# Kernel optimization log

Measured on AMD Instinct MI355X. Metric: run time of the kernel, lower is better.

The kernel has to match this reference:

```python
import jax, jax.numpy as jnp
import numpy as np

B, IN_DIM, HID, LAT, L, K = 65536, 512, 256, 64, 3, 2048


def setup_inputs() -> dict:
    key = jax.random.key(0)
    ks = jax.random.split(key, 10)
    s = 0.05
    return {
        "x": jax.random.normal(ks[0], (B, IN_DIM), jnp.float32),
        "enc_w1": jax.random.normal(ks[1], (IN_DIM, HID), jnp.float32) * s,
        "enc_b1": jnp.zeros((HID,), jnp.float32),
        "enc_w2": jax.random.normal(ks[2], (HID, LAT), jnp.float32) * s,
        "enc_b2": jnp.zeros((LAT,), jnp.float32),
        "codebooks": jax.random.normal(ks[3], (L, K, LAT), jnp.float32),
        "dec_w1": jax.random.normal(ks[4], (LAT, HID), jnp.float32) * s,
        "dec_b1": jnp.zeros((HID,), jnp.float32),
        "dec_w2": jax.random.normal(ks[5], (HID, IN_DIM), jnp.float32) * s,
        "dec_b2": jnp.zeros((IN_DIM,), jnp.float32),
    }


def reference(x, enc_w1, enc_b1, enc_w2, enc_b2, codebooks,
              dec_w1, dec_b1, dec_w2, dec_b2):
    # encoder: Linear -> ReLU -> Linear
    z = jax.nn.relu(x @ enc_w1 + enc_b1) @ enc_w2 + enc_b2  # [B, LAT]

    quantized = jnp.zeros_like(z)
    codes, residuals = [], []
    num_layers = codebooks.shape[0]
    for i in range(num_layers):  # small fixed layer loop (structurally sequential)
        residual = z - jax.lax.stop_gradient(quantized)  # [B, LAT]
        residuals.append(residual)
        C = codebooks[i]  # [K, LAT]
        # squared euclidean distances (argmin identical to cdist argmin)
        sqdist = (jnp.sum(residual * residual, axis=-1, keepdims=True)
                  - 2.0 * (residual @ C.T)
                  + jnp.sum(C * C, axis=-1))  # [B, K]
        code = jnp.argmin(sqdist, axis=-1)  # [B]
        codes.append(code)
        quantized = C[code] + jax.lax.stop_gradient(quantized)

    # decoder: Linear -> ReLU -> Linear
    x_recon = jax.nn.relu(quantized @ dec_w1 + dec_b1) @ dec_w2 + dec_b2  # [B, IN_DIM]
    return (jnp.stack(codes), x_recon, quantized, jnp.stack(residuals))
```

## Files before the change

### kernel.cpp

```cpp
#include <hip/hip_runtime.h>
#include <float.h>

#define NB      65536
#define IN_DIM  512
#define HID     256
#define LAT     64
#define NLAYERS 3
#define NK      2048
#define DELTA   1e-2f

typedef __attribute__((ext_vector_type(8)))  short s16x8;
typedef __attribute__((ext_vector_type(16))) float fp32x16;

__device__ __forceinline__ unsigned short f2bf(float v) {
  unsigned u = __float_as_uint(v);
  unsigned r = (u + 0x7fffu + ((u >> 16) & 1u)) >> 16;
  return (unsigned short)r;
}
__device__ __forceinline__ float bf2f(unsigned short h) {
  return __uint_as_float((unsigned)h << 16);
}

template<bool RELU>
__global__ __launch_bounds__(256) void gemm_f32(
    const float* __restrict__ A, const float* __restrict__ W,
    const float* __restrict__ bias, float* __restrict__ C,
    int M, int N, int K) {
  __shared__ float As[32][132];
  __shared__ float Bs[32][64];
  const int tid = threadIdx.x;
  const int cg  = tid & 15;
  const int rg  = tid >> 4;
  const int m0  = blockIdx.x * 128;
  const int n0  = blockIdx.y * 64;

  float acc[8][4];
#pragma unroll
  for (int i = 0; i < 8; ++i)
#pragma unroll
    for (int j = 0; j < 4; ++j) acc[i][j] = 0.f;

  for (int k0 = 0; k0 < K; k0 += 32) {
#pragma unroll
    for (int p = 0; p < 4; ++p) {
      int a = tid + p * 256;
      int row = a >> 3, kq = (a & 7) * 4;
      float4 v = *reinterpret_cast<const float4*>(&A[(size_t)(m0 + row) * K + k0 + kq]);
      As[kq + 0][row] = v.x; As[kq + 1][row] = v.y;
      As[kq + 2][row] = v.z; As[kq + 3][row] = v.w;
    }
#pragma unroll
    for (int p = 0; p < 2; ++p) {
      int a = tid + p * 256;
      int kk = a >> 4, nq = (a & 15) * 4;
      *reinterpret_cast<float4*>(&Bs[kk][nq]) =
          *reinterpret_cast<const float4*>(&W[(size_t)(k0 + kk) * N + n0 + nq]);
    }
    __syncthreads();
#pragma unroll
    for (int kk = 0; kk < 32; ++kk) {
      float4 a0 = *reinterpret_cast<const float4*>(&As[kk][rg * 8]);
      float4 a1 = *reinterpret_cast<const float4*>(&As[kk][rg * 8 + 4]);
      float4 b0 = *reinterpret_cast<const float4*>(&Bs[kk][cg * 4]);
      float av[8] = {a0.x, a0.y, a0.z, a0.w, a1.x, a1.y, a1.z, a1.w};
      float bv[4] = {b0.x, b0.y, b0.z, b0.w};
#pragma unroll
      for (int i = 0; i < 8; ++i)
#pragma unroll
        for (int j = 0; j < 4; ++j)
          acc[i][j] = fmaf(av[i], bv[j], acc[i][j]);
    }
    __syncthreads();
  }

  float4 bb = *reinterpret_cast<const float4*>(&bias[n0 + cg * 4]);
  float bv[4] = {bb.x, bb.y, bb.z, bb.w};
#pragma unroll
  for (int i = 0; i < 8; ++i) {
    float vals[4];
#pragma unroll
    for (int j = 0; j < 4; ++j) {
      float v = __fadd_rn(acc[i][j], bv[j]);
      if (RELU) v = fmaxf(v, 0.f);
      vals[j] = v;
    }
    float4 o; o.x = vals[0]; o.y = vals[1]; o.z = vals[2]; o.w = vals[3];
    *reinterpret_cast<float4*>(&C[(size_t)(m0 + rg * 8 + i) * N + n0 + cg * 4]) = o;
  }
}

template<bool RELU>
__global__ __launch_bounds__(256) void gemm128(
    const float* __restrict__ A, const float* __restrict__ W,
    const float* __restrict__ bias, float* __restrict__ C,
    int M, int N, int K) {
  __shared__ float As[16][132];
  __shared__ float Bs[16][132];
  const int tid  = threadIdx.x;
  const int cg   = tid & 15;
  const int rg   = tid >> 4;
  const int sw   = (cg >> 2) & 1;
  const int colA = cg * 8 + sw * 4;
  const int colB = cg * 8 + (sw ^ 1) * 4;
  const int m0   = blockIdx.x * 128;
  const int n0   = blockIdx.y * 128;

  const int arow = tid >> 2;
  const int akq  = (tid & 3) * 4;
  const int bk   = tid >> 5;
  const int bn   = (tid & 31) * 4;

  const float* Ap0 = A + (size_t)(m0 + arow) * K + akq;
  const float* Ap1 = A + (size_t)(m0 + arow + 64) * K + akq;
  const float* Wp0 = W + (size_t)bk * N + n0 + bn;
  const float* Wp1 = W + (size_t)(bk + 8) * N + n0 + bn;

  float acc[8][8];
#pragma unroll
  for (int i = 0; i < 8; ++i)
#pragma unroll
    for (int j = 0; j < 8; ++j) acc[i][j] = 0.f;

  float4 av0, av1, bv0, bv1;
  av0 = *reinterpret_cast<const float4*>(Ap0);
  av1 = *reinterpret_cast<const float4*>(Ap1);
  bv0 = *reinterpret_cast<const float4*>(Wp0);
  bv1 = *reinterpret_cast<const float4*>(Wp1);

  auto write_tile = [&]() {
    As[akq + 0][arow] = av0.x; As[akq + 1][arow] = av0.y;
    As[akq + 2][arow] = av0.z; As[akq + 3][arow] = av0.w;
    As[akq + 0][arow + 64] = av1.x; As[akq + 1][arow + 64] = av1.y;
    As[akq + 2][arow + 64] = av1.z; As[akq + 3][arow + 64] = av1.w;
    *reinterpret_cast<float4*>(&Bs[bk][bn])     = bv0;
    *reinterpret_cast<float4*>(&Bs[bk + 8][bn]) = bv1;
  };
  auto compute_tile = [&]() {
#pragma unroll
    for (int kk = 0; kk < 16; ++kk) {
      float4 a0 = *reinterpret_cast<const float4*>(&As[kk][rg * 8]);
      float4 a1 = *reinterpret_cast<const float4*>(&As[kk][rg * 8 + 4]);
      float4 b0 = *reinterpret_cast<const float4*>(&Bs[kk][colA]);
      float4 b1 = *reinterpret_cast<const float4*>(&Bs[kk][colB]);
      float rv[8] = {a0.x, a0.y, a0.z, a0.w, a1.x, a1.y, a1.z, a1.w};
      float cv[8] = {b0.x, b0.y, b0.z, b0.w, b1.x, b1.y, b1.z, b1.w};
#pragma unroll
      for (int i = 0; i < 8; ++i)
#pragma unroll
        for (int j = 0; j < 8; ++j)
          acc[i][j] = fmaf(rv[i], cv[j], acc[i][j]);
    }
  };

  write_tile();
  __syncthreads();
#pragma unroll 1
  for (int k0 = 16; k0 < K; k0 += 16) {
    av0 = *reinterpret_cast<const float4*>(Ap0 + k0);
    av1 = *reinterpret_cast<const float4*>(Ap1 + k0);
    bv0 = *reinterpret_cast<const float4*>(Wp0 + (size_t)k0 * N);
    bv1 = *reinterpret_cast<const float4*>(Wp1 + (size_t)k0 * N);
    compute_tile();
    __syncthreads();
    write_tile();
    __syncthreads();
  }
  compute_tile();

  float4 bA = *reinterpret_cast<const float4*>(&bias[n0 + colA]);
  float4 bB = *reinterpret_cast<const float4*>(&bias[n0 + colB]);
  float ba[8] = {bA.x, bA.y, bA.z, bA.w, bB.x, bB.y, bB.z, bB.w};
#pragma unroll
  for (int i = 0; i < 8; ++i) {
    size_t row = (size_t)(m0 + rg * 8 + i);
    float o[8];
#pragma unroll
    for (int j = 0; j < 8; ++j) {
      float v = __fadd_rn(acc[i][j], ba[j]);
      if (RELU) v = fmaxf(v, 0.f);
      o[j] = v;
    }
    float4 oA; oA.x = o[0]; oA.y = o[1]; oA.z = o[2]; oA.w = o[3];
    float4 oB; oB.x = o[4]; oB.y = o[5]; oB.z = o[6]; oB.w = o[7];
    *reinterpret_cast<float4*>(&C[row * N + n0 + colA]) = oA;
    *reinterpret_cast<float4*>(&C[row * N + n0 + colB]) = oB;
  }
}

__global__ void cnorm_f32(const float* __restrict__ cb, float* __restrict__ cn) {
  int i = blockIdx.x * blockDim.x + threadIdx.x;
  if (i >= NLAYERS * NK) return;
  const float* row = cb + (size_t)i * LAT;
  float r[8];
#pragma unroll
  for (int j = 0; j < 8; ++j) r[j] = 0.f;
#pragma unroll
  for (int t = 0; t < 8; ++t)
#pragma unroll
    for (int j = 0; j < 8; ++j) {
      float v = row[t * 8 + j];
      r[j] = __fadd_rn(r[j], __fmul_rn(v, v));
    }
  cn[i] = __fadd_rn(__fadd_rn(__fadd_rn(r[0], r[1]), __fadd_rn(r[2], r[3])),
                    __fadd_rn(__fadd_rn(r[4], r[5]), __fadd_rn(r[6], r[7])));
}

__global__ void split_cb(const float* __restrict__ cb,
                         unsigned short* __restrict__ cbf) {
  const int sid  = blockIdx.x * 256 + threadIdx.x;
  const int lane = sid & 63;
  const int grp  = sid >> 6;
  const int fg   = grp & 7;
  const int chl  = grp >> 3;
  const int nt = fg >> 2, ks = fg & 3;
  const int layer = chl >> 5, ch = chl & 31;
  const int code = ch * 64 + nt * 32 + (lane & 31);
  const int k0 = ks * 16 + (lane >> 5) * 8;
  const float* src = cb + ((size_t)layer * NK + code) * LAT + k0;
  float4 a = *(const float4*)src;
  float4 b = *(const float4*)(src + 4);
  float v[8] = {a.x, a.y, a.z, a.w, b.x, b.y, b.z, b.w};
  s16x8 hi, lo;
#pragma unroll
  for (int i = 0; i < 8; ++i) {
    unsigned short h = f2bf(v[i]);
    hi[i] = (short)h;
    lo[i] = (short)f2bf(__fsub_rn(v[i], bf2f(h)));
  }
  *(s16x8*)(cbf + ((size_t)grp * 2 + 0) * 512 + lane * 8) = hi;
  *(s16x8*)(cbf + ((size_t)grp * 2 + 1) * 512 + lane * 8) = lo;
}

__global__ void split_w(const float* __restrict__ W,
                        unsigned short* __restrict__ wf, int K, int N) {
  const int total = (K / 16) * (N / 32) * 64;
  const int idx = blockIdx.x * 256 + threadIdx.x;
  if (idx >= total) return;
  const int lane = idx & 63;
  const int grp  = idx >> 6;
  const int ntn  = N / 32;
  const int ks   = grp / ntn;
  const int ntg  = grp % ntn;
  const int col  = ntg * 32 + (lane & 31);
  const int k0   = ks * 16 + (lane >> 5) * 8;
  s16x8 hi, lo;
#pragma unroll
  for (int i = 0; i < 8; ++i) {
    float v = W[(size_t)(k0 + i) * N + col];
    unsigned short h = f2bf(v);
    hi[i] = (short)h;
    lo[i] = (short)f2bf(__fsub_rn(v, bf2f(h)));
  }
  *(s16x8*)(wf + ((size_t)grp * 2 + 0) * 512 + lane * 8) = hi;
  *(s16x8*)(wf + ((size_t)grp * 2 + 1) * 512 + lane * 8) = lo;
}

__global__ __launch_bounds__(256, 2) void rq_mfma(
    const float* __restrict__ zg,
    const float* __restrict__ cb,
    const unsigned short* __restrict__ cbf,
    const float* __restrict__ cnorm,
    float* __restrict__ out_codes,
    float* __restrict__ out_quant,
    float* __restrict__ out_res) {
  __shared__ unsigned short cbS[2][8192];
  __shared__ float cnSL[NK];
  __shared__ float m1S[128][2];
  __shared__ int   candS[128][8];
  __shared__ int   cntS[128][2];
  __shared__ int   flagS[128][2];
  __shared__ int   selS[128];
  __shared__ float rnS[128];
  __shared__ float bestD[256];
  __shared__ int   bestK[256];

  const int tid    = threadIdx.x;
  const int w      = tid >> 6;
  const int rgrp   = w >> 1;
  const int nthalf = w & 1;
  const int lane   = tid & 63;
  const int half   = lane >> 5;
  const int lcol   = lane & 31;
  const int rb0    = blockIdx.x * 128;

  s16x8 ah[2][4], al[2][4];

  for (int layer = 0; layer < NLAYERS; ++layer) {
    const float* cbL = cb + (size_t)layer * NK * LAT;
    const float* cnL = cnorm + (size_t)layer * NK;
    const unsigned short* cbfL = cbf + (size_t)layer * (NK * LAT * 2);
    float* resL = out_res + (size_t)layer * NB * LAT;

#pragma unroll
    for (int m = 0; m < 2; ++m) {
      const size_t row = (size_t)(rb0 + rgrp * 64 + m * 32 + lcol);
#pragma unroll
      for (int ks = 0; ks < 4; ++ks) {
        const int k0 = ks * 16 + half * 8;
        const float* zp = zg + row * LAT + k0;
        float4 a = *(const float4*)zp;
        float4 b = *(const float4*)(zp + 4);
        float r[8] = {a.x, a.y, a.z, a.w, b.x, b.y, b.z, b.w};
        if (layer > 0) {
          const float* qp = out_quant + row * LAT + k0;
          float4 qa = *(const float4*)qp;
          float4 qb = *(const float4*)(qp + 4);
          float q[8] = {qa.x, qa.y, qa.z, qa.w, qb.x, qb.y, qb.z, qb.w};
#pragma unroll
          for (int i = 0; i < 8; ++i) r[i] = __fsub_rn(r[i], q[i]);
          if (nthalf == 0) {
            float4 o0 = {r[0], r[1], r[2], r[3]};
            float4 o1 = {r[4], r[5], r[6], r[7]};
            *(float4*)(resL + row * LAT + k0) = o0;
            *(float4*)(resL + row * LAT + k0 + 4) = o1;
          }
        }
#pragma unroll
        for (int i = 0; i < 8; ++i) {
          unsigned short hh = f2bf(r[i]);
          float hf = bf2f(hh);
          ah[m][ks][i] = (short)hh;
          al[m][ks][i] = (short)f2bf(__fsub_rn(r[i], hf));
        }
      }
    }

    s16x8 stg[4];
#pragma unroll
    for (int p = 0; p < 4; ++p)
      stg[p] = *(const s16x8*)(cbfL + p * 2048 + tid * 8);
    float4 cn0 = *(const float4*)(cnL + tid * 8);
    float4 cn1 = *(const float4*)(cnL + tid * 8 + 4);
    __syncthreads();

#pragma unroll
    for (int p = 0; p < 4; ++p)
      *(s16x8*)(&cbS[0][p * 2048 + tid * 8]) = stg[p];
    *(float4*)(&cnSL[tid * 8])     = cn0;
    *(float4*)(&cnSL[tid * 8 + 4]) = cn1;
    if (tid < 128) {
      const float* rp = resL + (size_t)(rb0 + tid) * LAT;
      float r8[8] = {0.f, 0.f, 0.f, 0.f, 0.f, 0.f, 0.f, 0.f};
#pragma unroll
      for (int tb = 0; tb < 8; ++tb) {
        float4 x0 = *(const float4*)(rp + tb * 8);
        float4 x1 = *(const float4*)(rp + tb * 8 + 4);
        float v[8] = {x0.x, x0.y, x0.z, x0.w, x1.x, x1.y, x1.z, x1.w};
#pragma unroll
        for (int j = 0; j < 8; ++j)
          r8[j] = __fadd_rn(r8[j], __fmul_rn(v[j], v[j]));
      }
      rnS[tid] = __fadd_rn(
          __fadd_rn(__fadd_rn(r8[0], r8[1]), __fadd_rn(r8[2], r8[3])),
          __fadd_rn(__fadd_rn(r8[4], r8[5]), __fadd_rn(r8[6], r8[7])));
    }
    __syncthreads();

    float v1[2][16], v2[2][16];
    int   i1[2][16];
#pragma unroll
    for (int m = 0; m < 2; ++m)
#pragma unroll
      for (int r = 0; r < 16; ++r) {
        v1[m][r] = FLT_MAX; v2[m][r] = FLT_MAX; i1[m][r] = 0;
      }

#pragma unroll 1
    for (int ch = 0; ch < 32; ++ch) {
      const int buf = ch & 1;
      const bool haveNext = (ch + 1) < 32;
      if (haveNext) {
        const unsigned short* src = cbfL + (size_t)(ch + 1) * 8192;
#pragma unroll
        for (int p = 0; p < 4; ++p)
          stg[p] = *(const s16x8*)(src + p * 2048 + tid * 8);
      }

      s16x8 bh[4], bl[4];
#pragma unroll
      for (int ks = 0; ks < 4; ++ks) {
        bh[ks] = *(const s16x8*)(&cbS[buf][((nthalf * 4 + ks) * 2 + 0) * 512 + lane * 8]);
        bl[ks] = *(const s16x8*)(&cbS[buf][((nthalf * 4 + ks) * 2 + 1) * 512 + lane * 8]);
      }
      const int kbase = ch * 64 + nthalf * 32 + lcol;
      const float cnv = cnSL[kbase];

      fp32x16 acc0, acc1;
#pragma unroll
      for (int r = 0; r < 16; ++r) { acc0[r] = 0.f; acc1[r] = 0.f; }
#pragma unroll
      for (int ks = 0; ks < 4; ++ks) {
        acc0 = __builtin_amdgcn_mfma_f32_32x32x16_bf16(ah[0][ks], bh[ks], acc0, 0, 0, 0);
        acc1 = __builtin_amdgcn_mfma_f32_32x32x16_bf16(ah[1][ks], bh[ks], acc1, 0, 0, 0);
        acc0 = __builtin_amdgcn_mfma_f32_32x32x16_bf16(ah[0][ks], bl[ks], acc0, 0, 0, 0);
        acc1 = __builtin_amdgcn_mfma_f32_32x32x16_bf16(ah[1][ks], bl[ks], acc1, 0, 0, 0);
        acc0 = __builtin_amdgcn_mfma_f32_32x32x16_bf16(al[0][ks], bh[ks], acc0, 0, 0, 0);
        acc1 = __builtin_amdgcn_mfma_f32_32x32x16_bf16(al[1][ks], bh[ks], acc1, 0, 0, 0);
      }

#pragma unroll
      for (int r = 0; r < 16; ++r) {
        {
          float d = fmaf(-2.f, acc0[r], cnv);
          float nv2 = fminf(fmaxf(d, v1[0][r]), v2[0][r]);
          bool c = d < v1[0][r];
          i1[0][r] = c ? kbase : i1[0][r];
          v1[0][r] = fminf(v1[0][r], d);
          v2[0][r] = nv2;
        }
        {
          float d = fmaf(-2.f, acc1[r], cnv);
          float nv2 = fminf(fmaxf(d, v1[1][r]), v2[1][r]);
          bool c = d < v1[1][r];
          i1[1][r] = c ? kbase : i1[1][r];
          v1[1][r] = fminf(v1[1][r], d);
          v2[1][r] = nv2;
        }
      }

      if (haveNext) {
#pragma unroll
        for (int p = 0; p < 4; ++p)
          *(s16x8*)(&cbS[buf ^ 1][p * 2048 + tid * 8]) = stg[p];
      }
      __syncthreads();
    }

#pragma unroll
    for (int m = 0; m < 2; ++m)
#pragma unroll
      for (int r = 0; r < 16; ++r) {
        float m1 = v1[m][r];
        m1 = fminf(m1, __shfl_xor(m1, 1));
        m1 = fminf(m1, __shfl_xor(m1, 2));
        m1 = fminf(m1, __shfl_xor(m1, 4));
        m1 = fminf(m1, __shfl_xor(m1, 8));
        m1 = fminf(m1, __shfl_xor(m1, 16));
        const int rowloc = rgrp * 64 + m * 32 + (r & 3) + 8 * (r >> 2) + 4 * half;
        if (lcol == 0) m1S[rowloc][nthalf] = m1;
      }
    __syncthreads();
#pragma unroll
    for (int m = 0; m < 2; ++m)
#pragma unroll
      for (int r = 0; r < 16; ++r) {
        const int rowloc = rgrp * 64 + m * 32 + (r & 3) + 8 * (r >> 2) + 4 * half;
        float thr = fminf(m1S[rowloc][0], m1S[rowloc][1]) + DELTA;
        unsigned long long bc = __ballot(v1[m][r] <= thr);
        unsigned long long bf = __ballot(v2[m][r] <= thr);
        unsigned mc = (unsigned)(bc >> (half * 32));
        unsigned mf = (unsigned)(bf >> (half * 32));
        int pos = __popc(mc & ((1u << lcol) - 1u));
        if (v1[m][r] <= thr && pos < 4) candS[rowloc][nthalf * 4 + pos] = i1[m][r];
        if (lcol == 0) {
          int c = __popc(mc);
          cntS[rowloc][nthalf]  = (c < 4) ? c : 4;
          flagS[rowloc][nthalf] = (mf != 0u) || (c > 4);
        }
      }
    __syncthreads();

    if (tid < 128) {
      const int t = tid;
      if ((flagS[t][0] | flagS[t][1]) == 0) {
        const float* rp = resL + (size_t)(rb0 + t) * LAT;
        float rr[64];
#pragma unroll
        for (int j = 0; j < 16; ++j) {
          float4 x = *(const float4*)(rp + j * 4);
          rr[j * 4 + 0] = x.x; rr[j * 4 + 1] = x.y;
          rr[j * 4 + 2] = x.z; rr[j * 4 + 3] = x.w;
        }
        const float rn = rnS[t];
        float bd = FLT_MAX; int bk = 0x7fffffff;
        const int c0 = cntS[t][0], c1n = cntS[t][1];
        for (int c = 0; c < c0 + c1n; ++c) {
          int k = candS[t][(c < c0) ? c : (4 + c - c0)];
          const float* cp = cbL + (size_t)k * LAT;
          float dot = 0.f;
#pragma unroll
          for (int j = 0; j < 64; ++j) dot = fmaf(rr[j], cp[j], dot);
          float d = __fadd_rn(__fsub_rn(rn, __fmul_rn(2.f, dot)), cnL[k]);
          if (d < bd || (d == bd && k < bk)) { bd = d; bk = k; }
        }
        selS[t] = bk;
        out_codes[(size_t)layer * NB + rb0 + t] = (float)bk;
      }
    }
    __syncthreads();

#pragma unroll 1
    for (int t2 = 0; t2 < 128; ++t2) {
      if ((flagS[t2][0] | flagS[t2][1]) == 0) continue;
      const float* rp = resL + (size_t)(rb0 + t2) * LAT;
      const float rn = rnS[t2];
      float bd = FLT_MAX; int bk = 0x7fffffff;
#pragma unroll 1
      for (int j = 0; j < 8; ++j) {
        int k = tid * 8 + j;
        const float* cp = cbL + (size_t)k * LAT;
        float dot = 0.f;
        for (int q = 0; q < 64; ++q) dot = fmaf(rp[q], cp[q], dot);
        float d = __fadd_rn(__fsub_rn(rn, __fmul_rn(2.f, dot)), cnL[k]);
        if (d < bd || (d == bd && k < bk)) { bd = d; bk = k; }
      }
      bestD[tid] = bd; bestK[tid] = bk;
      __syncthreads();
      if (tid == 0) {
        float gd = FLT_MAX; int gk = 0x7fffffff;
        for (int i = 0; i < 256; ++i) {
          float d = bestD[i]; int k = bestK[i];
          if (d < gd || (d == gd && k < gk)) { gd = d; gk = k; }
        }
        selS[t2] = gk;
        out_codes[(size_t)layer * NB + rb0 + t2] = (float)gk;
      }
      __syncthreads();
    }

    if (nthalf == 0) {
#pragma unroll
      for (int m = 0; m < 2; ++m) {
        const int rowloc = rgrp * 64 + m * 32 + lcol;
        const size_t row = (size_t)(rb0 + rowloc);
        const int sel = selS[rowloc];
        const float* cp = cbL + (size_t)sel * LAT;
#pragma unroll
        for (int ks = 0; ks < 4; ++ks) {
          const int k0 = ks * 16 + half * 8;
          float4 c0 = *(const float4*)(cp + k0);
          float4 c1 = *(const float4*)(cp + k0 + 4);
          float* qp = out_quant + row * LAT + k0;
          if (layer == 0) {
            *(float4*)qp = c0; *(float4*)(qp + 4) = c1;
          } else {
            float4 q0 = *(const float4*)qp;
            float4 q1 = *(const float4*)(qp + 4);
            q0.x = __fadd_rn(c0.x, q0.x); q0.y = __fadd_rn(c0.y, q0.y);
            q0.z = __fadd_rn(c0.z, q0.z); q0.w = __fadd_rn(c0.w, q0.w);
            q1.x = __fadd_rn(c1.x, q1.x); q1.y = __fadd_rn(c1.y, q1.y);
            q1.z = __fadd_rn(c1.z, q1.z); q1.w = __fadd_rn(c1.w, q1.w);
            *(float4*)qp = q0; *(float4*)(qp + 4) = q1;
          }
        }
      }
    }
    __syncthreads();
  }
}

__global__ __launch_bounds__(256) void dec1_mfma(
    const float* __restrict__ q, const unsigned short* __restrict__ wf,
    const float* __restrict__ bias,
    unsigned short* __restrict__ h_hi, unsigned short* __restrict__ h_lo) {
  const int tid  = threadIdx.x;
  const int w    = tid >> 6;
  const int lane = tid & 63;
  const int half = lane >> 5;
  const int lcol = lane & 31;
  const int m0   = blockIdx.x * 128 + w * 32;
  const int n0   = blockIdx.y * 128;

  fp32x16 acc[4];
#pragma unroll
  for (int nt = 0; nt < 4; ++nt)
#pragma unroll
    for (int r = 0; r < 16; ++r) acc[nt][r] = 0.f;

  const size_t arow = (size_t)(m0 + lcol);
#pragma unroll
  for (int ks = 0; ks < 4; ++ks) {
    const float* ap = q + arow * LAT + ks * 16 + half * 8;
    float4 a0 = *(const float4*)ap;
    float4 a1 = *(const float4*)(ap + 4);
    float av[8] = {a0.x, a0.y, a0.z, a0.w, a1.x, a1.y, a1.z, a1.w};
    s16x8 ah, al;
#pragma unroll
    for (int i = 0; i < 8; ++i) {
      unsigned short hh = f2bf(av[i]);
      ah[i] = (short)hh;
      al[i] = (short)f2bf(__fsub_rn(av[i], bf2f(hh)));
    }
#pragma unroll
    for (int nt = 0; nt < 4; ++nt) {
      const int grp = ks * 8 + (blockIdx.y * 4 + nt);
      const unsigned short* base = wf + (size_t)grp * 1024;
      s16x8 bh = *(const s16x8*)(base + lane * 8);
      s16x8 bl = *(const s16x8*)(base + 512 + lane * 8);
      acc[nt] = __builtin_amdgcn_mfma_f32_32x32x16_bf16(ah, bh, acc[nt], 0, 0, 0);
      acc[nt] = __builtin_amdgcn_mfma_f32_32x32x16_bf16(ah, bl, acc[nt], 0, 0, 0);
      acc[nt] = __builtin_amdgcn_mfma_f32_32x32x16_bf16(al, bh, acc[nt], 0, 0, 0);
    }
  }

#pragma unroll
  for (int nt = 0; nt < 4; ++nt) {
    const int col = n0 + nt * 32 + lcol;
    const float b = bias[col];
#pragma unroll
    for (int r = 0; r < 16; ++r) {
      const int rowo = (r & 3) + 8 * (r >> 2) + 4 * half;
      const size_t grow = (size_t)(m0 + rowo);
      float v = fmaxf(__fadd_rn(acc[nt][r], b), 0.f);
      unsigned short hh = f2bf(v);
      h_hi[grow * HID + col] = hh;
      h_lo[grow * HID + col] = f2bf(__fsub_rn(v, bf2f(hh)));
    }
  }
}

__global__ __launch_bounds__(256) void dec2_mfma(
    const unsigned short* __restrict__ h_hi,
    const unsigned short* __restrict__ h_lo,
    const unsigned short* __restrict__ wf,
    const float* __restrict__ bias, float* __restrict__ C) {
  const int tid  = threadIdx.x;
  const int w    = tid >> 6;
  const int lane = tid & 63;
  const int half = lane >> 5;
  const int lcol = lane & 31;
  const int m0   = blockIdx.x * 128 + w * 32;
  const int n0   = blockIdx.y * 128;

  fp32x16 acc[4];
#pragma unroll
  for (int nt = 0; nt < 4; ++nt)
#pragma unroll
    for (int r = 0; r < 16; ++r) acc[nt][r] = 0.f;

  const size_t arow = (size_t)(m0 + lcol);
#pragma unroll 1
  for (int ks = 0; ks < 16; ++ks) {
    const size_t aoff = arow * HID + ks * 16 + half * 8;
    s16x8 ah = *(const s16x8*)(h_hi + aoff);
    s16x8 al = *(const s16x8*)(h_lo + aoff);
#pragma unroll
    for (int nt = 0; nt < 4; ++nt) {
      const int grp = ks * 16 + (blockIdx.y * 4 + nt);
      const unsigned short* base = wf + (size_t)grp * 1024;
      s16x8 bh = *(const s16x8*)(base + lane * 8);
      s16x8 bl = *(const s16x8*)(base + 512 + lane * 8);
      acc[nt] = __builtin_amdgcn_mfma_f32_32x32x16_bf16(ah, bh, acc[nt], 0, 0, 0);
      acc[nt] = __builtin_amdgcn_mfma_f32_32x32x16_bf16(ah, bl, acc[nt], 0, 0, 0);
      acc[nt] = __builtin_amdgcn_mfma_f32_32x32x16_bf16(al, bh, acc[nt], 0, 0, 0);
    }
  }

#pragma unroll
  for (int nt = 0; nt < 4; ++nt) {
    const int col = n0 + nt * 32 + lcol;
    const float b = bias[col];
#pragma unroll
    for (int r = 0; r < 16; ++r) {
      const int rowo = (r & 3) + 8 * (r >> 2) + 4 * half;
      C[(size_t)(m0 + rowo) * IN_DIM + col] = __fadd_rn(acc[nt][r], b);
    }
  }
}

extern "C" void kernel_launch(void* const* d_in, const int* in_sizes, int n_in,
                              void* d_out, int out_size, void* d_ws, size_t ws_size,
                              hipStream_t stream) {
  (void)in_sizes; (void)n_in; (void)out_size;
  const float* x   = (const float*)d_in[0];
  const float* ew1 = (const float*)d_in[1];
  const float* eb1 = (const float*)d_in[2];
  const float* ew2 = (const float*)d_in[3];
  const float* eb2 = (const float*)d_in[4];
  const float* cbk = (const float*)d_in[5];
  const float* dw1 = (const float*)d_in[6];
  const float* db1 = (const float*)d_in[7];
  const float* dw2 = (const float*)d_in[8];
  const float* db2 = (const float*)d_in[9];

  float* out     = (float*)d_out;
  float* o_codes = out;
  float* o_xrec  = out + (size_t)NLAYERS * NB;
  float* o_quant = o_xrec + (size_t)NB * IN_DIM;
  float* o_res   = o_quant + (size_t)NB * LAT;

  char* ws = (char*)d_ws;
  float* h            = (float*)ws;
  unsigned short* hhi = (unsigned short*)ws;
  unsigned short* hlo = (unsigned short*)(ws + (size_t)32 * 1024 * 1024);
  float* cn           = (float*)(ws + (size_t)64 * 1024 * 1024);
  unsigned short* w1f = (unsigned short*)(ws + (size_t)64 * 1024 * 1024 + 32768);
  unsigned short* w2f = (unsigned short*)(ws + (size_t)64 * 1024 * 1024 + 32768 + 65536);
  const size_t ws_need = (size_t)64 * 1024 * 1024 + 32768 + 65536 + 524288;
  const bool fast_dec = ws_size >= ws_need;

  unsigned short* cbf = (unsigned short*)(o_xrec + (size_t)16 * 1024 * 1024);

  cnorm_f32<<<(NLAYERS * NK + 255) / 256, 256, 0, stream>>>(cbk, cn);
  split_cb<<<192, 256, 0, stream>>>(cbk, cbf);
  if (fast_dec) {
    split_w<<<((LAT / 16) * (HID / 32) * 64 + 255) / 256, 256, 0, stream>>>(dw1, w1f, LAT, HID);
    split_w<<<((HID / 16) * (IN_DIM / 32) * 64 + 255) / 256, 256, 0, stream>>>(dw2, w2f, HID, IN_DIM);
  }
  gemm128<true ><<<dim3(NB / 128, HID / 128), 256, 0, stream>>>(x, ew1, eb1, h,     NB, HID, IN_DIM);
  gemm_f32<false><<<dim3(NB / 128, LAT / 64),  256, 0, stream>>>(h, ew2, eb2, o_res, NB, LAT, HID);
  rq_mfma<<<NB / 128, 256, 0, stream>>>(o_res, cbk, cbf, cn, o_codes, o_quant, o_res);
  if (fast_dec) {
    dec1_mfma<<<dim3(NB / 128, 2), 256, 0, stream>>>(o_quant, w1f, db1, hhi, hlo);
    dec2_mfma<<<dim3(NB / 128, 4), 256, 0, stream>>>(hhi, hlo, w2f, db2, o_xrec);
  } else {
    gemm128<true ><<<dim3(NB / 128, HID / 128),    256, 0, stream>>>(o_quant, dw1, db1, h,      NB, HID,    LAT);
    gemm128<false><<<dim3(NB / 128, IN_DIM / 128), 256, 0, stream>>>(h,       dw2, db2, o_xrec, NB, IN_DIM, HID);
  }
}
```

Measured before the change: 694.1 us.

## Stream codebook fragments directly from global into registers, dropping LDS staging

Removes the LDS double buffer and per-chunk __syncthreads in the codebook scan. Each wave now loads its MFMA B fragments straight from global/L2 into registers, ping-ponging between two register sets. The -2 scale is folded into the pre-split codebook, the main and correction products go into separate accumulators that are added at the end, and v2 is updated with fmed3. This trades block-wide barriers and LDS traffic for more global/L2 loads, since both wave halves per row group now fetch fragments independently, and for higher register pressure.

Measured after the change: 884.2 us. 27.4% more time.

```diff
diff --git a/kernel.cpp b/kernel.cpp
--- a/kernel.cpp
+++ b/kernel.cpp
@@ -223,9 +223,10 @@
   s16x8 hi, lo;
 #pragma unroll
   for (int i = 0; i < 8; ++i) {
-    unsigned short h = f2bf(v[i]);
+    float nv = __fmul_rn(-2.f, v[i]);
+    unsigned short h = f2bf(nv);
     hi[i] = (short)h;
-    lo[i] = (short)f2bf(__fsub_rn(v[i], bf2f(h)));
+    lo[i] = (short)f2bf(__fsub_rn(nv, bf2f(h)));
   }
   *(s16x8*)(cbf + ((size_t)grp * 2 + 0) * 512 + lane * 8) = hi;
   *(s16x8*)(cbf + ((size_t)grp * 2 + 1) * 512 + lane * 8) = lo;
@@ -263,7 +264,6 @@
     float* __restrict__ out_codes,
     float* __restrict__ out_quant,
     float* __restrict__ out_res) {
-  __shared__ unsigned short cbS[2][8192];
   __shared__ float cnSL[NK];
   __shared__ float m1S[128][2];
   __shared__ int   candS[128][8];
@@ -284,6 +284,10 @@
   const int rb0    = blockIdx.x * 128;
 
   s16x8 ah[2][4], al[2][4];
+
+  fp32x16 Z;
+#pragma unroll
+  for (int r = 0; r < 16; ++r) Z[r] = 0.f;
 
   for (int layer = 0; layer < NLAYERS; ++layer) {
     const float* cbL = cb + (size_t)layer * NK * LAT;
@@ -325,17 +329,10 @@
       }
     }
 
-    s16x8 stg[4];
-#pragma unroll
-    for (int p = 0; p < 4; ++p)
-      stg[p] = *(const s16x8*)(cbfL + p * 2048 + tid * 8);
     float4 cn0 = *(const float4*)(cnL + tid * 8);
     float4 cn1 = *(const float4*)(cnL + tid * 8 + 4);
     __syncthreads();
 
-#pragma unroll
-    for (int p = 0; p < 4; ++p)
-      *(s16x8*)(&cbS[0][p * 2048 + tid * 8]) = stg[p];
     *(float4*)(&cnSL[tid * 8])     = cn0;
     *(float4*)(&cnSL[tid * 8 + 4]) = cn1;
     if (tid < 128) {
@@ -365,65 +362,48 @@
         v1[m][r] = FLT_MAX; v2[m][r] = FLT_MAX; i1[m][r] = 0;
       }
 
-#pragma unroll 1
-    for (int ch = 0; ch < 32; ++ch) {
-      const int buf = ch & 1;
-      const bool haveNext = (ch + 1) < 32;
-      if (haveNext) {
-        const unsigned short* src = cbfL + (size_t)(ch + 1) * 8192;
-#pragma unroll
-        for (int p = 0; p < 4; ++p)
-          stg[p] = *(const s16x8*)(src + p * 2048 + tid * 8);
-      }
-
-      s16x8 bh[4], bl[4];
+    s16x8 bhA[4], blA[4], bhB[4], blB[4];
+    auto loadF = [&](int ch, s16x8* BH, s16x8* BL) {
+      const unsigned short* base =
+          cbfL + (size_t)ch * 8192 + nthalf * 4096 + lane * 8;
 #pragma unroll
       for (int ks = 0; ks < 4; ++ks) {
-        bh[ks] = *(const s16x8*)(&cbS[buf][((nthalf * 4 + ks) * 2 + 0) * 512 + lane * 8]);
-        bl[ks] = *(const s16x8*)(&cbS[buf][((nthalf * 4 + ks) * 2 + 1) * 512 + lane * 8]);
-      }
+        BH[ks] = *(const s16x8*)(base + ks * 1024);
+        BL[ks] = *(const s16x8*)(base + ks * 1024 + 512);
+      }
+    };
+    auto computeF = [&](int ch, const s16x8* BH, const s16x8* BL) {
       const int kbase = ch * 64 + nthalf * 32 + lcol;
       const float cnv = cnSL[kbase];
-
-      fp32x16 acc0, acc1;
-#pragma unroll
-      for (int r = 0; r < 16; ++r) { acc0[r] = 0.f; acc1[r] = 0.f; }
-#pragma unroll
-      for (int ks = 0; ks < 4; ++ks) {
-        acc0 = __builtin_amdgcn_mfma_f32_32x32x16_bf16(ah[0][ks], bh[ks], acc0, 0, 0, 0);
-        acc1 = __builtin_amdgcn_mfma_f32_32x32x16_bf16(ah[1][ks], bh[ks], acc1, 0, 0, 0);
-        acc0 = __builtin_amdgcn_mfma_f32_32x32x16_bf16(ah[0][ks], bl[ks], acc0, 0, 0, 0);
-        acc1 = __builtin_amdgcn_mfma_f32_32x32x16_bf16(ah[1][ks], bl[ks], acc1, 0, 0, 0);
-        acc0 = __builtin_amdgcn_mfma_f32_32x32x16_bf16(al[0][ks], bh[ks], acc0, 0, 0, 0);
-        acc1 = __builtin_amdgcn_mfma_f32_32x32x16_bf16(al[1][ks], bh[ks], acc1, 0, 0, 0);
-      }
-
-#pragma unroll
-      for (int r = 0; r < 16; ++r) {
-        {
-          float d = fmaf(-2.f, acc0[r], cnv);
-          float nv2 = fminf(fmaxf(d, v1[0][r]), v2[0][r]);
-          bool c = d < v1[0][r];
-          i1[0][r] = c ? kbase : i1[0][r];
-          v1[0][r] = fminf(v1[0][r], d);
-          v2[0][r] = nv2;
-        }
-        {
-          float d = fmaf(-2.f, acc1[r], cnv);
-          float nv2 = fminf(fmaxf(d, v1[1][r]), v2[1][r]);
-          bool c = d < v1[1][r];
-          i1[1][r] = c ? kbase : i1[1][r];
-          v1[1][r] = fminf(v1[1][r], d);
-          v2[1][r] = nv2;
-        }
-      }
-
-      if (haveNext) {
-#pragma unroll
-        for (int p = 0; p < 4; ++p)
-          *(s16x8*)(&cbS[buf ^ 1][p * 2048 + tid * 8]) = stg[p];
-      }
-      __syncthreads();
+#pragma unroll
+      for (int m = 0; m < 2; ++m) {
+        fp32x16 aA = Z, aB = Z;
+#pragma unroll
+        for (int ks = 0; ks < 4; ++ks)
+          aA = __builtin_amdgcn_mfma_f32_32x32x16_bf16(ah[m][ks], BH[ks], aA, 0, 0, 0);
+#pragma unroll
+        for (int ks = 0; ks < 4; ++ks) {
+          aB = __builtin_amdgcn_mfma_f32_32x32x16_bf16(ah[m][ks], BL[ks], aB, 0, 0, 0);
+          aB = __builtin_amdgcn_mfma_f32_32x32x16_bf16(al[m][ks], BH[ks], aB, 0, 0, 0);
+        }
+#pragma unroll
+        for (int r = 0; r < 16; ++r) {
+          float d = __fadd_rn(cnv, __fadd_rn(aA[r], aB[r]));
+          v2[m][r] = __builtin_amdgcn_fmed3f(d, v1[m][r], v2[m][r]);
+          bool c = d < v1[m][r];
+          i1[m][r] = c ? kbase : i1[m][r];
+          v1[m][r] = fminf(v1[m][r], d);
+        }
+      }
+    };
+
+    loadF(0, bhA, blA);
+#pragma unroll 1
+    for (int ch = 0; ch < 32; ch += 2) {
+      loadF(ch + 1, bhB, blB);
+      computeF(ch, bhA, blA);
+      if (ch + 2 < 32) loadF(ch + 2, bhA, blA);
+      computeF(ch + 1, bhB, blB);
     }
 
 #pragma unroll
```
